# Performance work log

Measured on AMD Instinct MI355X. Metric: run time of the kernel, lower is better.

Reference implementation:

```python
import jax, jax.numpy as jnp
from jax import lax
import numpy as np

B = 256
EMB_DIM = 64
N_EMB = 512
LAT1 = 1024   # 16 slots * 64
LAT2 = 512
LAT = LAT1 + LAT2  # 1536
COMMIT = 0.25
EMB_COST = 1.0


def setup_inputs() -> dict:
    key = jax.random.key(0)
    ks = iter(jax.random.split(key, 40))

    def w(shape, fan_in):
        return jax.random.normal(next(ks), shape, jnp.float32) * np.float32(1.0 / np.sqrt(fan_in))

    def b(n):
        return jax.random.normal(next(ks), (n,), jnp.float32) * np.float32(0.01)

    inp = {}
    inp['x'] = jax.random.normal(next(ks), (B, 3, 64, 64), jnp.float32)
    # encoder convs, torch OIHW layout, k=4
    inp['ew0'] = w((64, 3, 4, 4), 3 * 16);   inp['eb0'] = b(64)
    inp['ew1'] = w((64, 64, 4, 4), 64 * 16); inp['eb1'] = b(64)
    inp['ew2'] = w((128, 64, 4, 4), 64 * 16); inp['eb2'] = b(128)
    inp['ew3'] = w((256, 128, 4, 4), 128 * 16); inp['eb3'] = b(256)
    # encoder fc11: 4096 -> 1024 -> 1024 -> 1536, stored (in,out)
    inp['fw0'] = w((4096, 1024), 4096); inp['fb0'] = b(1024)
    inp['fw1'] = w((1024, 1024), 1024); inp['fb1'] = b(1024)
    inp['fw2'] = w((1024, LAT), 1024);  inp['fb2'] = b(LAT)
    # VQ codebook
    inp['codebook'] = jax.random.normal(next(ks), (N_EMB, EMB_DIM), jnp.float32)
    # decoder fc3: 1536 -> 512 -> 1024 -> 4096
    inp['gw0'] = w((LAT, 512), LAT);    inp['gb0'] = b(512)
    inp['gw1'] = w((512, 1024), 512);   inp['gb1'] = b(1024)
    inp['gw2'] = w((1024, 4096), 1024); inp['gb2'] = b(4096)
    # decoder ConvTranspose2d weights, torch layout (Cin, Cout, kh, kw)
    inp['tw0'] = w((256, 128, 4, 4), 256 * 16); inp['tb0'] = b(128)
    inp['tw1'] = w((128, 64, 4, 4), 128 * 16);  inp['tb1'] = b(64)
    inp['tw2'] = w((64, 64, 4, 4), 64 * 16);    inp['tb2'] = b(64)
    inp['tw3'] = w((64, 3, 4, 4), 64 * 16);     inp['tb3'] = b(3)
    return inp


def _conv(x, w, b):
    # Conv2d k=4 s=2 p=1 -> halves H,W
    y = lax.conv_general_dilated(x, w, (2, 2), ((1, 1), (1, 1)),
                                 dimension_numbers=('NCHW', 'OIHW', 'NCHW'))
    return y + b[None, :, None, None]


def _convt(x, w, b):
    # ConvTranspose2d k=4 s=2 p=1 -> doubles H,W.
    # Equivalent to lhs_dilation=2, pad k-1-p=2, flipped kernel, swapped I/O.
    wf = jnp.flip(w, (2, 3)).transpose(1, 0, 2, 3)
    y = lax.conv_general_dilated(x, wf, (1, 1), ((2, 2), (2, 2)),
                                 lhs_dilation=(2, 2),
                                 dimension_numbers=('NCHW', 'OIHW', 'NCHW'))
    return y + b[None, :, None, None]


def _forward(x, ew0, eb0, ew1, eb1, ew2, eb2, ew3, eb3,
             fw0, fb0, fw1, fb1, fw2, fb2, codebook,
             gw0, gb0, gw1, gb1, gw2, gb2,
             tw0, tb0, tw1, tb1, tw2, tb2, tw3, tb3):
    relu = jax.nn.relu
    # --- encoder conv stack (last conv has no ReLU) ---
    h = relu(_conv(x, ew0, eb0))
    h = relu(_conv(h, ew1, eb1))
    h = relu(_conv(h, ew2, eb2))
    h = _conv(h, ew3, eb3)                      # [B,256,4,4]
    h = h.reshape(h.shape[0], -1)               # [B,4096]
    h = relu(h @ fw0 + fb0)
    h = relu(h @ fw1 + fb1)
    z = h @ fw2 + fb2                           # [B,1536]
    # --- split content / style (isVQStyle=False) ---
    z_c = z[:, :LAT1]
    z_s = z[:, LAT1:]
    # --- vector quantize z_c (16 slots of dim 64, shared codebook) ---
    flat = z_c.reshape(-1, EMB_DIM)             # [B*16, 64]
    d = (jnp.sum(flat * flat, axis=1, keepdims=True)
         + jnp.sum(codebook * codebook, axis=1)
         - 2.0 * flat @ codebook.T)             # [B*16, 512]
    idx = jnp.argmin(d, axis=1)
    quantized = codebook[idx].reshape(z_c.shape)  # [B,1024]
    sg = lax.stop_gradient
    q_latent_loss = jnp.mean((quantized - sg(z_c)) ** 2) * EMB_COST
    e_latent_loss = jnp.mean((z_c - sg(quantized)) ** 2) * COMMIT
    loss = q_latent_loss + e_latent_loss
    quantized = z_c + sg(quantized - z_c)       # straight-through
    e = jnp.concatenate([quantized, z_s], axis=-1)  # [B,1536]
    # --- decoder ---
    g = relu(e @ gw0 + gb0)
    g = relu(g @ gw1 + gb1)
    g = (g @ gw2 + gb2).reshape(-1, 256, 4, 4)
    g = relu(_convt(g, tw0, tb0))
    g = relu(_convt(g, tw1, tb1))
    g = relu(_convt(g, tw2, tb2))
    x_recon = _convt(g, tw3, tb3)               # [B,3,64,64]
    return x_recon, loss


def reference(x, ew0, eb0, ew1, eb1, ew2, eb2, ew3, eb3,
              fw0, fb0, fw1, fb1, fw2, fb2, codebook,
              gw0, gb0, gw1, gb1, gw2, gb2,
              tw0, tb0, tw1, tb1, tw2, tb2, tw3, tb3):
    return _forward(x, ew0, eb0, ew1, eb1, ew2, eb2, ew3, eb3,
                    fw0, fb0, fw1, fb1, fw2, fb2, codebook,
                    gw0, gb0, gw1, gb1, gw2, gb2,
                    tw0, tb0, tw1, tb1, tw2, tb2, tw3, tb3)
```

## Files before the change

### kernel.cpp

```cpp
#include <hip/hip_runtime.h>
#include <hip/hip_bf16.h>


#define TPB 256
typedef __attribute__((ext_vector_type(8))) short short8v;
typedef __attribute__((ext_vector_type(4))) float f32x4;
typedef unsigned int u32;
typedef unsigned short u16;

__device__ inline u16 f2bf(float x){
  union { __hip_bfloat16 b; u16 u; } cv;
  cv.b = __float2bfloat16(x);
  return cv.u;
}
__device__ inline float bf2f(u16 h){ union{u32 u;float f;}v; v.u=((u32)h)<<16; return v.f;}
__device__ inline u32 packhl(float x){ u16 h=f2bf(x); u16 l=f2bf(x-bf2f(h)); return ((u32)l<<16)|(u32)h;}

template<int NS>
__device__ inline void splitN(float x, u16 t[3]) {
  u16 h0 = f2bf(x); t[0] = h0;
  float r1 = x - bf2f(h0);
  u16 h1 = f2bf(r1); t[1] = h1;
  if (NS == 3) { float r2 = r1 - bf2f(h1); t[2] = f2bf(r2); }
}

template<int NS, int ST>
__device__ inline void stW(u32* L, int row, int oct, const u16 hs[3][8]) {
  constexpr int SWM = (ST == 64) ? 15 : 7;
  const int sw = row & SWM;
#pragma unroll
  for (int s = 0; s < NS; ++s) {
    uint4 d;
    d.x = (u32)hs[s][0] | ((u32)hs[s][1] << 16);
    d.y = (u32)hs[s][2] | ((u32)hs[s][3] << 16);
    d.z = (u32)hs[s][4] | ((u32)hs[s][5] << 16);
    d.w = (u32)hs[s][6] | ((u32)hs[s][7] << 16);
    int ch = (((s << 2) | oct) ^ sw) << 2;
    *reinterpret_cast<uint4*>(&L[row * ST + ch]) = d;
  }
}

template<int NS, int ST>
__device__ inline void stWf(u32* L, int row, int oct, const float v[8]) {
  u16 hs[3][8];
#pragma unroll
  for (int e = 0; e < 8; ++e) {
    u16 t3[3]; splitN<NS>(v[e], t3);
    hs[0][e] = t3[0]; hs[1][e] = t3[1]; if (NS == 3) hs[2][e] = t3[2];
  }
  stW<NS, ST>(L, row, oct, hs);
}

template<int ST>
__device__ inline void stWp(u32* L, int row, int oct, int s, uint4 d) {
  constexpr int SWM = (ST == 64) ? 15 : 7;
  int ch = (((s << 2) | oct) ^ (row & SWM)) << 2;
  *reinterpret_cast<uint4*>(&L[row * ST + ch]) = d;
}

template<int ST>
__device__ inline short8v rdFrag(const u32* L, int row, int c) {
  constexpr int SWM = (ST == 64) ? 15 : 7;
  int ph = (c ^ (row & SWM)) << 2;
  return *reinterpret_cast<const short8v*>(&L[row * ST + ph]);
}

__global__ __launch_bounds__(TPB) void wsplit3_k(
    const float* __restrict__ src, u16* __restrict__ dst, int n)
{
  for (int i = blockIdx.x * TPB + threadIdx.x; i < n; i += gridDim.x * TPB) {
    u16 t3[3]; splitN<3>(src[i], t3);
    dst[i] = t3[0]; dst[i + n] = t3[1]; dst[i + 2 * n] = t3[2];
  }
}
__global__ __launch_bounds__(TPB) void wprep2_k(
    const float* __restrict__ src, u16* __restrict__ dh, u16* __restrict__ dl,
    int Ci, int Co)
{
  int K4 = Ci << 2;
  int tot = 4 * Co * K4;
  for (int i = blockIdx.x * TPB + threadIdx.x; i < tot; i += gridDim.x * TPB) {
    int par = i / (Co * K4); int rem = i - par * (Co * K4);
    int co = rem / K4; int k4 = rem - co * K4;
    int ci = k4 >> 2, ay = (k4 >> 1) & 1, ax = k4 & 1;
    int py = par >> 1, px = par & 1;
    int widx = ((1 - py) << 2) + (1 - px) + (ay << 3) + (ax << 1);
    float x = src[(((size_t)ci * Co + co) << 4) + widx];
    u16 h = f2bf(x);
    dh[i] = h; dl[i] = f2bf(x - bf2f(h));
  }
}

__global__ __launch_bounds__(TPB) void x_pad_k(
    const float* __restrict__ x, float* __restrict__ xp)
{
  int idx = blockIdx.x * TPB + threadIdx.x;
  if (idx >= 3345408) return;
  int px = idx % 66; int t = idx / 66; int py = t % 66; int p = t / 66;
  float v = 0.f;
  if (py >= 1 && py <= 64 && px >= 1 && px <= 64)
    v = x[(size_t)p * 4096 + (py - 1) * 64 + (px - 1)];
  xp[idx] = v;
}
__global__ __launch_bounds__(TPB) void zb0_k(float* __restrict__ h0p)
{
  int idx = blockIdx.x * TPB + threadIdx.x;
  if (idx >= 2162688) return;
  int p = idx / 132, k = idx % 132;
  int py, px;
  if (k < 34)       { py = 0;           px = k; }
  else if (k < 68)  { py = 33;          px = k - 34; }
  else if (k < 100) { py = k - 68 + 1;  px = 0; }
  else              { py = k - 100 + 1; px = 33; }
  h0p[(size_t)p * 1156 + py * 34 + px] = 0.f;
}

template<int RM, int OUTM>
__global__ __launch_bounds__(TPB, 2) void conv_ad(
    const float* __restrict__ in, const u16* __restrict__ wsp,
    const float* __restrict__ bias, float* __restrict__ outp,
    int Ci, int Co, int Wi, int lwo, int relu, int KSPL, int PS,
    int bS, int ciS, int Mtot)
{
  constexpr int BM = RM * 64;
  __shared__ __align__(16) u32 BL[2][64 * 64];
  const int K = Ci << 4;
  const int PW = Wi + 2;
  const int Wo = Wi >> 1;
  const int tid = threadIdx.x;
  const int m0 = blockIdx.x * BM, n0 = blockIdx.y << 6;
  const int lane = tid & 63, wv = tid >> 6, r = lane & 15, g = lane >> 4;
  const int kb0 = blockIdx.z * KSPL;
  const int kbN = min(kb0 + KSPL, K);
  const int khsel = g & 1;
  const int cig = g >> 1;
  f32x4 acc[RM][4] = {};

  int base[RM];
#pragma unroll
  for (int mm = 0; mm < RM; ++mm) {
    int cell = m0 + (wv * RM + mm) * 16 + r;
    int x = cell & (Wo - 1), y = (cell >> lwo) & (Wo - 1), b = cell >> (lwo + lwo);
    base[mm] = b * bS + (2 * y + 2 * khsel) * PW + 2 * x;
  }

  auto gA = [&](int kb, float v[RM][8]) {
    if ((kb + (g << 3)) < K) {
      int cioff = ((kb >> 4) + cig) * ciS;
#pragma unroll
      for (int mm = 0; mm < RM; ++mm) {
        const float* p = in + base[mm] + cioff;
#pragma unroll
        for (int e = 0; e < 8; ++e)
          v[mm][e] = p[(e >> 2) * PW + (e & 3)];
      }
    } else {
#pragma unroll
      for (int mm = 0; mm < RM; ++mm)
#pragma unroll
        for (int e = 0; e < 8; ++e) v[mm][e] = 0.f;
    }
  };
  auto gB = [&](int kb, uint4* d) {
    int n = tid & 63, oc2 = tid >> 6;
    int k8 = kb + (oc2 << 3);
    if (k8 < K) {
      const u16* wp = wsp + (size_t)(n0 + n) * K + k8;
      d[0] = *reinterpret_cast<const uint4*>(wp);
      d[1] = *reinterpret_cast<const uint4*>(wp + PS);
      d[2] = *reinterpret_cast<const uint4*>(wp + 2 * PS);
    } else {
      d[0] = d[1] = d[2] = make_uint4(0u, 0u, 0u, 0u);
    }
  };
  auto mkfrags = [&](const float v[8], short8v f[3]) {
    u16 hs[3][8];
#pragma unroll
    for (int e = 0; e < 8; ++e) {
      u16 t3[3]; splitN<3>(v[e], t3);
      hs[0][e] = t3[0]; hs[1][e] = t3[1]; hs[2][e] = t3[2];
    }
#pragma unroll
    for (int s = 0; s < 3; ++s) {
      union { u16 u[8]; short8v sv; } cv;
#pragma unroll
      for (int e = 0; e < 8; ++e) cv.u[e] = hs[s][e];
      f[s] = cv.sv;
    }
  };

  float vA[RM][8], vA2[RM][8];
  uint4 vB[3], vB2[3];
  gA(kb0, vA); gB(kb0, vB);
  for (int kb = kb0; kb < kbN; kb += 32) {
    u32* BLc = BL[((kb - kb0) >> 5) & 1];
    {
      int n = tid & 63, oc2 = tid >> 6;
      stWp<64>(BLc, n, oc2, 0, vB[0]);
      stWp<64>(BLc, n, oc2, 1, vB[1]);
      stWp<64>(BLc, n, oc2, 2, vB[2]);
    }
    const bool more = (kb + 32) < kbN;
    if (more) { gB(kb + 32, vB2); gA(kb + 32, vA2); }
    short8v a_[RM][3];
#pragma unroll
    for (int mm = 0; mm < RM; ++mm) mkfrags(vA[mm], a_[mm]);
    __syncthreads();
#pragma unroll
    for (int ns = 0; ns < 4; ++ns) {
      short8v b_[3];
#pragma unroll
      for (int s = 0; s < 3; ++s) b_[s] = rdFrag<64>(BLc, (ns << 4) + r, (s << 2) | g);
#pragma unroll
      for (int mm = 0; mm < RM; ++mm) {
        acc[mm][ns] = __builtin_amdgcn_mfma_f32_16x16x32_bf16(a_[mm][0], b_[0], acc[mm][ns], 0, 0, 0);
        acc[mm][ns] = __builtin_amdgcn_mfma_f32_16x16x32_bf16(a_[mm][0], b_[1], acc[mm][ns], 0, 0, 0);
        acc[mm][ns] = __builtin_amdgcn_mfma_f32_16x16x32_bf16(a_[mm][1], b_[0], acc[mm][ns], 0, 0, 0);
        acc[mm][ns] = __builtin_amdgcn_mfma_f32_16x16x32_bf16(a_[mm][1], b_[1], acc[mm][ns], 0, 0, 0);
        acc[mm][ns] = __builtin_amdgcn_mfma_f32_16x16x32_bf16(a_[mm][0], b_[2], acc[mm][ns], 0, 0, 0);
        acc[mm][ns] = __builtin_amdgcn_mfma_f32_16x16x32_bf16(a_[mm][2], b_[0], acc[mm][ns], 0, 0, 0);
      }
    }
    if (more) {
#pragma unroll
      for (int mm = 0; mm < RM; ++mm)
#pragma unroll
        for (int e = 0; e < 8; ++e) vA[mm][e] = vA2[mm][e];
#pragma unroll
      for (int s = 0; s < 3; ++s) vB[s] = vB2[s];
    }
  }
#pragma unroll
  for (int mm = 0; mm < RM; ++mm)
#pragma unroll
    for (int ns = 0; ns < 4; ++ns) {
      int c0 = m0 + (wv * RM + mm) * 16 + (g << 2);
      int co = n0 + (ns << 4) + r;
      if (OUTM == 0) {
        float bv = bias[co];
        const int OPW = Wo + 2;
        const int OPHW = OPW * OPW;
#pragma unroll
        for (int q = 0; q < 4; ++q) {
          int cell = c0 + q;
          int x = cell & (Wo - 1), y = (cell >> lwo) & (Wo - 1), b = cell >> (lwo + lwo);
          float v = acc[mm][ns][q] + bv;
          if (relu) v = fmaxf(v, 0.f);
          outp[((size_t)(b * Co + co)) * OPHW + (y + 1) * OPW + (x + 1)] = v;
        }
      } else {
        float4 o;
        o.x = acc[mm][ns][0]; o.y = acc[mm][ns][1];
        o.z = acc[mm][ns][2]; o.w = acc[mm][ns][3];
        *reinterpret_cast<float4*>(
            &outp[((size_t)(blockIdx.z * Co + co)) * Mtot + c0]) = o;
      }
    }
}

__global__ __launch_bounds__(TPB) void combine_cm_k(
    const float* __restrict__ P, const float* __restrict__ bias,
    float* __restrict__ out)
{
  int idx = blockIdx.x * TPB + threadIdx.x;
  if (idx >= 5308416) return;
  int px = idx % 18; int t = idx / 18; int py = t % 18; t /= 18;
  int b = t % 256; int co = t / 256;
  float v = 0.f;
  if (py >= 1 && py <= 16 && px >= 1 && px <= 16) {
    int cell = b * 256 + (py - 1) * 16 + (px - 1);
    v = P[(size_t)co * 65536 + cell] + P[(size_t)(64 + co) * 65536 + cell] + bias[co];
    v = fmaxf(v, 0.f);
  }
  out[idx] = v;
}

__global__ __launch_bounds__(TPB) void combine_pad_k(
    const float* __restrict__ P, const float* __restrict__ bias,
    float* __restrict__ out)
{
  int idx = blockIdx.x * TPB + threadIdx.x;
  if (idx >= 3276800) return;
  int px = idx % 10; int t = idx / 10; int py = t % 10; t /= 10;
  int co = t % 128; int b = t / 128;
  float v = 0.f;
  if (py >= 1 && py <= 8 && px >= 1 && px <= 8) {
    int cell = b * 64 + (py - 1) * 8 + (px - 1);
    float s = 0.f;
#pragma unroll
    for (int z = 0; z < 4; ++z)
      s += P[((size_t)(z * 128 + co)) * 16384 + cell];
    v = fmaxf(s + bias[co], 0.f);
  }
  out[idx] = v;
}

__global__ __launch_bounds__(TPB) void conv_combine(
    const float* __restrict__ P, const float* __restrict__ bias,
    float* __restrict__ out, int Mtot, int N, int SK, int lwo, int relu)
{
  int idx = blockIdx.x * TPB + threadIdx.x;
  int mq = Mtot >> 2;
  int co = idx / mq;
  int cell0 = (idx - co * mq) << 2;
  if (co >= N) return;
  float4 s = make_float4(0.f, 0.f, 0.f, 0.f);
  for (int z = 0; z < SK; ++z) {
    const float4 pv = *reinterpret_cast<const float4*>(
        &P[((size_t)z * N + co) * Mtot + cell0]);
    s.x += pv.x; s.y += pv.y; s.z += pv.z; s.w += pv.w;
  }
  float bv = bias[co];
  s.x += bv; s.y += bv; s.z += bv; s.w += bv;
  if (relu) { s.x = fmaxf(s.x, 0.f); s.y = fmaxf(s.y, 0.f);
              s.z = fmaxf(s.z, 0.f); s.w = fmaxf(s.w, 0.f); }
  int Wo = 1 << lwo;
  int x = cell0 & (Wo - 1), y = (cell0 >> lwo) & (Wo - 1), b = cell0 >> (lwo + lwo);
  *reinterpret_cast<float4*>(&out[(((size_t)b * N + co) * Wo + y) * Wo + x]) = s;
}

template<int NS, int OUTM>
__global__ __launch_bounds__(TPB) void gemm_mf(
    const float* __restrict__ A, const float* __restrict__ W,
    const float* __restrict__ bias, void* __restrict__ outp,
    int M, int K, int N, int KSPL)
{
  constexpr int ST = (NS == 3) ? 64 : 32;
  __shared__ __align__(16) u32 L[(64 + 64) * ST];
  u32* AL = L; u32* BL = L + 64 * ST;
  const int tid = threadIdx.x;
  const int m0 = blockIdx.x << 6, n0 = blockIdx.y << 6;
  const int lane = tid & 63, wv = tid >> 6, r = lane & 15, g = lane >> 4;
  const int kb0 = blockIdx.z * KSPL;
  const int kbN = kb0 + KSPL;
  const int cl = tid & 63, oct = tid >> 6;
  f32x4 acc[4] = {};

  float vA[8], vB[8], vA2[8], vB2[8];
  auto gA = [&](int kt, float* v) {
    const float* ap = &A[(size_t)(m0 + cl) * K + kt + (oct << 3)];
    *reinterpret_cast<float4*>(&v[0]) = *reinterpret_cast<const float4*>(ap);
    *reinterpret_cast<float4*>(&v[4]) = *reinterpret_cast<const float4*>(ap + 4);
  };
  auto gB = [&](int kt, float* v) {
#pragma unroll
    for (int e = 0; e < 8; ++e)
      v[e] = W[(size_t)(kt + (oct << 3) + e) * N + n0 + cl];
  };

  gA(kb0, vA); gB(kb0, vB);
  for (int kt = kb0; kt < kbN; kt += 32) {
    const bool more = (kt + 32) < kbN;
    if (more) { gA(kt + 32, vA2); gB(kt + 32, vB2); }
    stWf<NS, ST>(AL, cl, oct, vA);
    stWf<NS, ST>(BL, cl, oct, vB);
    __syncthreads();
    short8v a_[3];
#pragma unroll
    for (int s = 0; s < NS; ++s) a_[s] = rdFrag<ST>(AL, (wv << 4) + r, (s << 2) | g);
#pragma unroll
    for (int ns = 0; ns < 4; ++ns) {
      short8v b_[3];
#pragma unroll
      for (int s = 0; s < NS; ++s) b_[s] = rdFrag<ST>(BL, (ns << 4) + r, (s << 2) | g);
      acc[ns] = __builtin_amdgcn_mfma_f32_16x16x32_bf16(a_[0], b_[0], acc[ns], 0, 0, 0);
      acc[ns] = __builtin_amdgcn_mfma_f32_16x16x32_bf16(a_[0], b_[1], acc[ns], 0, 0, 0);
      acc[ns] = __builtin_amdgcn_mfma_f32_16x16x32_bf16(a_[1], b_[0], acc[ns], 0, 0, 0);
      if (NS == 3) {
        acc[ns] = __builtin_amdgcn_mfma_f32_16x16x32_bf16(a_[1], b_[1], acc[ns], 0, 0, 0);
        acc[ns] = __builtin_amdgcn_mfma_f32_16x16x32_bf16(a_[0], b_[2], acc[ns], 0, 0, 0);
        acc[ns] = __builtin_amdgcn_mfma_f32_16x16x32_bf16(a_[2], b_[0], acc[ns], 0, 0, 0);
      }
    }
    __syncthreads();
    if (more) {
#pragma unroll
      for (int e = 0; e < 8; ++e) { vA[e] = vA2[e]; vB[e] = vB2[e]; }
    }
  }
#pragma unroll
  for (int ns = 0; ns < 4; ++ns)
#pragma unroll
    for (int q = 0; q < 4; ++q) {
      int m = m0 + (wv << 4) + (g << 2) + q;
      int n = n0 + (ns << 4) + r;
      float v = acc[ns][q];
      if (OUTM == 0) ((float*)outp)[((size_t)blockIdx.z * M + m) * N + n] = v;
      else           ((u32*)outp)[(size_t)m * N + n] = packhl(v + bias[n]);
    }
}

__global__ __launch_bounds__(TPB) void combine_k(
    const float* __restrict__ P, const float* __restrict__ bias,
    float* __restrict__ out, int MN, int N, int SK, int relu)
{
  int i4 = (blockIdx.x * TPB + threadIdx.x) << 2;
  if (i4 >= MN) return;
  float4 s = make_float4(0.f, 0.f, 0.f, 0.f);
  for (int z = 0; z < SK; ++z) {
    const float4 pv = *reinterpret_cast<const float4*>(&P[(size_t)z * MN + i4]);
    s.x += pv.x; s.y += pv.y; s.z += pv.z; s.w += pv.w;
  }
  int n = i4 % N;
  s.x += bias[n]; s.y += bias[n + 1]; s.z += bias[n + 2]; s.w += bias[n + 3];
  if (relu) { s.x = fmaxf(s.x, 0.f); s.y = fmaxf(s.y, 0.f);
              s.z = fmaxf(s.z, 0.f); s.w = fmaxf(s.w, 0.f); }
  *reinterpret_cast<float4*>(&out[i4]) = s;
}

__global__ __launch_bounds__(TPB) void combine_pk_k(
    const float* __restrict__ P, const float* __restrict__ bias,
    u32* __restrict__ out)
{
  int i4 = (blockIdx.x * TPB + threadIdx.x) << 2;
  if (i4 >= 1048576) return;
  const float4 p0 = *reinterpret_cast<const float4*>(&P[i4]);
  const float4 p1 = *reinterpret_cast<const float4*>(&P[1048576 + i4]);
  int n = i4 % 4096;
  uint4 o;
  o.x = packhl(p0.x + p1.x + bias[n]);
  o.y = packhl(p0.y + p1.y + bias[n + 1]);
  o.z = packhl(p0.z + p1.z + bias[n + 2]);
  o.w = packhl(p0.w + p1.w + bias[n + 3]);
  *reinterpret_cast<uint4*>(&out[i4]) = o;
}

template<int BM, int EMIT, int SPLITIN>
__global__ __launch_bounds__(TPB) void convt_mf2(
    const u32* __restrict__ in, const u16* __restrict__ wth,
    const u16* __restrict__ wtl, const float* __restrict__ bias,
    u32* __restrict__ outq, int Ci, int Co, int Hi, int lwi, int relu)
{
  constexpr int ST = 32, MS = BM / 64;
  constexpr int STC = BM + 4;
  constexpr int LSZ = ((BM + 64) * ST > 64 * STC) ? (BM + 64) * ST : 64 * STC;
  __shared__ __align__(16) u32 L[LSZ];
  u32* AL = L; u32* BL = L + BM * ST;
  const int Wi = Hi, K4 = Ci << 2;
  const int HW = Hi * Wi, HWq = HW >> 2, Wiq = Wi >> 1;
  const int par = blockIdx.z, py = par >> 1, px = par & 1;
  const int tid = threadIdx.x;
  const int m0 = blockIdx.x * BM, n0 = blockIdx.y << 6;
  const int lane = tid & 63, wv = tid >> 6, r = lane & 15, g = lane >> 4;
  f32x4 acc[MS][4] = {};

  const int cl  = (BM == 128) ? (tid & 127) : (tid & 63);
  const int oc0 = (BM == 128) ? (tid >> 7) : (tid >> 6);
  int offT[4]; u32 mskT[4];
  {
    int cell = m0 + cl;
    int X = cell & (Wi - 1), Y = (cell >> lwi) & (Wi - 1), b = cell >> (lwi + lwi);
#pragma unroll
    for (int t = 0; t < 4; ++t) {
      int ay = t >> 1, ax = t & 1;
      int gy = Y + py - ay, gx = X + px - ax;
      bool ok = (gy >= 0 && gy < Hi && gx >= 0 && gx < Wi);
      int gyc = min(max(gy, 0), Hi - 1), gxc = min(max(gx, 0), Wi - 1);
      if (SPLITIN) {
        int q = ((gyc & 1) << 1) | (gxc & 1);
        offT[t] = q * (256 * Ci * HWq) + b * Ci * HWq + (gyc >> 1) * Wiq + (gxc >> 1);
      } else {
        offT[t] = b * Ci * HW + gyc * Wi + gxc;
      }
      mskT[t] = ok ? 0xffffffffu : 0u;
    }
  }
  const int stepCi = SPLITIN ? HWq : HW;

  auto gA = [&](int kb, u32 v[][8]) {
#pragma unroll
    for (int p = 0; p < MS; ++p) {
      int oc = oc0 + (p << 1);
      int cibase = ((kb >> 2) + (oc << 1)) * stepCi;
#pragma unroll
      for (int e = 0; e < 8; ++e) {
        int t = e & 3;
        v[p][e] = in[offT[t] + cibase + ((e >> 2) ? stepCi : 0)] & mskT[t];
      }
    }
  };
  auto gB = [&](int kb, uint4* d) {
    int n = tid & 63, oc2 = tid >> 6;
    size_t base = (size_t)(par * Co + n0 + n) * K4 + kb + (oc2 << 3);
    d[0] = *reinterpret_cast<const uint4*>(wth + base);
    d[1] = *reinterpret_cast<const uint4*>(wtl + base);
  };

  u32 vA[MS][8], vA2[MS][8];
  uint4 vB[2], vB2[2];
  gA(0, vA); gB(0, vB);
  for (int kb = 0; kb < K4; kb += 32) {
    const bool more = (kb + 32) < K4;
    if (more) { gA(kb + 32, vA2); gB(kb + 32, vB2); }
#pragma unroll
    for (int p = 0; p < MS; ++p) {
      const u32* v = vA[p];
      const int sw = cl & 7;
      int oc = oc0 + (p << 1);
      uint4 dh, dl;
      dh.x = (v[0] & 0xffffu) | (v[1] << 16);  dl.x = (v[0] >> 16) | (v[1] & 0xffff0000u);
      dh.y = (v[2] & 0xffffu) | (v[3] << 16);  dl.y = (v[2] >> 16) | (v[3] & 0xffff0000u);
      dh.z = (v[4] & 0xffffu) | (v[5] << 16);  dl.z = (v[4] >> 16) | (v[5] & 0xffff0000u);
      dh.w = (v[6] & 0xffffu) | (v[7] << 16);  dl.w = (v[6] >> 16) | (v[7] & 0xffff0000u);
      *reinterpret_cast<uint4*>(&AL[cl * ST + ((oc ^ sw) << 2)]) = dh;
      *reinterpret_cast<uint4*>(&AL[cl * ST + (((4 | oc) ^ sw) << 2)]) = dl;
    }
    {
      int n = tid & 63, oc2 = tid >> 6;
      stWp<ST>(BL, n, oc2, 0, vB[0]);
      stWp<ST>(BL, n, oc2, 1, vB[1]);
    }
    __syncthreads();
    short8v a_[MS][2];
#pragma unroll
    for (int mm = 0; mm < MS; ++mm)
#pragma unroll
      for (int s = 0; s < 2; ++s)
        a_[mm][s] = rdFrag<ST>(AL, (wv * MS + mm) * 16 + r, (s << 2) | g);
#pragma unroll
    for (int ns = 0; ns < 4; ++ns) {
      short8v b_[2];
#pragma unroll
      for (int s = 0; s < 2; ++s) b_[s] = rdFrag<ST>(BL, (ns << 4) + r, (s << 2) | g);
#pragma unroll
      for (int mm = 0; mm < MS; ++mm) {
        acc[mm][ns] = __builtin_amdgcn_mfma_f32_16x16x32_bf16(a_[mm][0], b_[0], acc[mm][ns], 0, 0, 0);
        acc[mm][ns] = __builtin_amdgcn_mfma_f32_16x16x32_bf16(a_[mm][0], b_[1], acc[mm][ns], 0, 0, 0);
        acc[mm][ns] = __builtin_amdgcn_mfma_f32_16x16x32_bf16(a_[mm][1], b_[0], acc[mm][ns], 0, 0, 0);
      }
    }
    __syncthreads();
    if (more) {
#pragma unroll
      for (int p = 0; p < MS; ++p)
#pragma unroll
        for (int e = 0; e < 8; ++e) vA[p][e] = vA2[p][e];
      vB[0] = vB2[0]; vB[1] = vB2[1];
    }
  }
#pragma unroll
  for (int mm = 0; mm < MS; ++mm)
#pragma unroll
    for (int ns = 0; ns < 4; ++ns)
#pragma unroll
      for (int q = 0; q < 4; ++q) {
        int cell = (wv * MS + mm) * 16 + (g << 2) + q;
        int col = (ns << 4) + r;
        float v = acc[mm][ns][q] + bias[n0 + col];
        if (relu) v = fmaxf(v, 0.f);
        L[col * STC + cell] = EMIT ? packhl(v) : __float_as_uint(v);
      }
  __syncthreads();
  const size_t QO = (size_t)256 * Co * HW;
  u32* op = outq + (size_t)par * QO;
  constexpr int C4N = BM / 4;
  constexpr int NCH = (BM * 64) / (TPB * 4);
#pragma unroll
  for (int it = 0; it < NCH; ++it) {
    int lin = it * TPB + tid;
    int c4 = lin & (C4N - 1);
    int col = lin / C4N;
    int cell0 = c4 << 2;
    uint4 d = *reinterpret_cast<const uint4*>(&L[col * STC + cell0]);
    int gc = m0 + cell0;
    int Xo = gc & (Wi - 1), Yo = (gc >> lwi) & (Wi - 1), bo = gc >> (lwi + lwi);
    *reinterpret_cast<uint4*>(
        &op[((size_t)(bo * Co + n0 + col) * Hi + Yo) * Wi + Xo]) = d;
  }
}

__global__ __launch_bounds__(TPB) void convt3_kernel(
    const float* __restrict__ inq, const float* __restrict__ w,
    float* __restrict__ part)
{
  __shared__ float wl[3072];
  __shared__ float il[8][33 * 32];
  const int b = blockIdx.x;
  const int z = blockIdx.y;
  const int tid = threadIdx.x;
  for (int i = tid; i < 3072; i += TPB) wl[i] = w[i];
  const int Y = tid >> 3;
  const int X0 = (tid & 7) << 2;
  float acc[3][2][8];
#pragma unroll
  for (int o = 0; o < 3; ++o)
#pragma unroll
    for (int p = 0; p < 2; ++p)
#pragma unroll
      for (int q = 0; q < 8; ++q) acc[o][p][q] = 0.f;

  const int cbeg = z << 5, cend = cbeg + 32;
  for (int c0 = cbeg; c0 < cend; c0 += 8) {
    __syncthreads();
    for (int i = tid; i < 8192; i += TPB) {
      int cc = i >> 10, yy = (i >> 5) & 31, xx = i & 31;
      int q = ((yy & 1) << 1) | (xx & 1);
      il[cc][yy * 33 + xx] = inq[(size_t)q * 4194304 +
          (((size_t)b * 64 + c0 + cc) * 16 + (yy >> 1)) * 16 + (xx >> 1)];
    }
    __syncthreads();
    for (int cc = 0; cc < 8; ++cc) {
      float iv[3][6];
#pragma unroll
      for (int j = 0; j < 3; ++j) {
        int gy = Y - 1 + j;
        int gyc = min(max(gy, 0), 31);
        float my = (gy >= 0 && gy < 32) ? 1.f : 0.f;
#pragma unroll
        for (int k = 0; k < 6; ++k) {
          int gx = X0 - 1 + k;
          int gxc = min(max(gx, 0), 31);
          float mx = (gx >= 0 && gx < 32) ? 1.f : 0.f;
          iv[j][k] = il[cc][gyc * 33 + gxc] * (my * mx);
        }
      }
      const float* wq = &wl[(c0 + cc) * 48];
#pragma unroll
      for (int o = 0; o < 3; ++o) {
        const float* wo = wq + o * 16;
#pragma unroll
        for (int c = 0; c < 4; ++c) {
          acc[o][0][2*c]   = fmaf(iv[1][c+1], wo[5],  acc[o][0][2*c]);
          acc[o][0][2*c]   = fmaf(iv[1][c],   wo[7],  acc[o][0][2*c]);
          acc[o][0][2*c]   = fmaf(iv[0][c+1], wo[13], acc[o][0][2*c]);
          acc[o][0][2*c]   = fmaf(iv[0][c],   wo[15], acc[o][0][2*c]);
          acc[o][0][2*c+1] = fmaf(iv[1][c+2], wo[4],  acc[o][0][2*c+1]);
          acc[o][0][2*c+1] = fmaf(iv[1][c+1], wo[6],  acc[o][0][2*c+1]);
          acc[o][0][2*c+1] = fmaf(iv[0][c+2], wo[12], acc[o][0][2*c+1]);
          acc[o][0][2*c+1] = fmaf(iv[0][c+1], wo[14], acc[o][0][2*c+1]);
          acc[o][1][2*c]   = fmaf(iv[2][c+1], wo[1],  acc[o][1][2*c]);
          acc[o][1][2*c]   = fmaf(iv[2][c],   wo[3],  acc[o][1][2*c]);
          acc[o][1][2*c]   = fmaf(iv[1][c+1], wo[9],  acc[o][1][2*c]);
          acc[o][1][2*c]   = fmaf(iv[1][c],   wo[11], acc[o][1][2*c]);
          acc[o][1][2*c+1] = fmaf(iv[2][c+2], wo[0],  acc[o][1][2*c+1]);
          acc[o][1][2*c+1] = fmaf(iv[2][c+1], wo[2],  acc[o][1][2*c+1]);
          acc[o][1][2*c+1] = fmaf(iv[1][c+2], wo[8],  acc[o][1][2*c+1]);
          acc[o][1][2*c+1] = fmaf(iv[1][c+1], wo[10], acc[o][1][2*c+1]);
        }
      }
    }
  }
  float* pz = part + (size_t)z * 3145728;
#pragma unroll
  for (int o = 0; o < 3; ++o) {
#pragma unroll
    for (int p = 0; p < 2; ++p) {
      float* op = pz + (((size_t)b * 3 + o) * 64 + 2 * Y + p) * 64 + 2 * X0;
      *reinterpret_cast<float4*>(op) =
          make_float4(acc[o][p][0], acc[o][p][1], acc[o][p][2], acc[o][p][3]);
      *reinterpret_cast<float4*>(op + 4) =
          make_float4(acc[o][p][4], acc[o][p][5], acc[o][p][6], acc[o][p][7]);
    }
  }
}

__global__ __launch_bounds__(TPB) void c3_combine(
    const float* __restrict__ part, const float* __restrict__ bias,
    float* __restrict__ out)
{
  int i4 = (blockIdx.x * TPB + threadIdx.x) << 2;
  const float4 p0 = *reinterpret_cast<const float4*>(&part[i4]);
  const float4 p1 = *reinterpret_cast<const float4*>(&part[i4 + 3145728]);
  int o = (i4 >> 12) % 3;
  float bv = bias[o];
  float4 s = make_float4(p0.x + p1.x + bv, p0.y + p1.y + bv,
                         p0.z + p1.z + bv, p0.w + p1.w + bv);
  *reinterpret_cast<float4*>(&out[i4]) = s;
}

__global__ __launch_bounds__(TPB) void vq_kernel(
    const float* __restrict__ z, const float* __restrict__ cb,
    float* __restrict__ e, float* __restrict__ rowloss)
{
  const int row = blockIdx.x;
  const int b = row >> 4, s = row & 15;
  __shared__ float zr[64];
  __shared__ float bval[TPB];
  __shared__ int   bidx[TPB];
  const int tid = threadIdx.x;
  if (tid < 64) zr[tid] = z[(size_t)b * 1536 + s * 64 + tid];
  __syncthreads();

  float best = 3.4e38f;
  int bi = 0;
#pragma unroll
  for (int rep = 0; rep < 2; ++rep) {
    int j = tid + rep * TPB;
    const float4* c4 = reinterpret_cast<const float4*>(cb + (size_t)j * 64);
    float d = 0.f;
#pragma unroll
    for (int k = 0; k < 16; ++k) {
      float4 cv = c4[k];
      float t0 = zr[4 * k + 0] - cv.x;
      float t1 = zr[4 * k + 1] - cv.y;
      float t2 = zr[4 * k + 2] - cv.z;
      float t3 = zr[4 * k + 3] - cv.w;
      d = fmaf(t0, t0, d); d = fmaf(t1, t1, d);
      d = fmaf(t2, t2, d); d = fmaf(t3, t3, d);
    }
    if (d < best) { best = d; bi = j; }
  }
  bval[tid] = best; bidx[tid] = bi;
  __syncthreads();
  for (int sft = 128; sft > 0; sft >>= 1) {
    if (tid < sft) {
      float v2 = bval[tid + sft]; int i2 = bidx[tid + sft];
      if (v2 < bval[tid] || (v2 == bval[tid] && i2 < bidx[tid])) {
        bval[tid] = v2; bidx[tid] = i2;
      }
    }
    __syncthreads();
  }
  const int bj = bidx[0];
  if (tid < 64)
    e[(size_t)b * 1536 + s * 64 + tid] = cb[(size_t)bj * 64 + tid];
  if (tid == 0) rowloss[row] = bval[0];
}

__global__ __launch_bounds__(TPB) void zs_copy_kernel(
    const float* __restrict__ z, float* __restrict__ e)
{
  int i = blockIdx.x * TPB + threadIdx.x;
  int b = i >> 9, k = i & 511;
  e[(size_t)b * 1536 + 1024 + k] = z[(size_t)b * 1536 + 1024 + k];
}

__global__ __launch_bounds__(TPB) void loss_reduce_kernel(
    const float* __restrict__ rl, float* __restrict__ out)
{
  __shared__ float sm[TPB];
  float s = 0.f;
  for (int i = threadIdx.x; i < 4096; i += TPB) s += rl[i];
  sm[threadIdx.x] = s;
  __syncthreads();
  for (int sft = 128; sft > 0; sft >>= 1) {
    if (threadIdx.x < sft) sm[threadIdx.x] += sm[threadIdx.x + sft];
    __syncthreads();
  }
  if (threadIdx.x == 0) out[0] = sm[0] * (1.25f / 262144.f);
}

extern "C" void kernel_launch(void* const* d_in, const int* in_sizes, int n_in,
                              void* d_out, int out_size, void* d_ws, size_t ws_size,
                              hipStream_t stream)
{
  const float* x    = (const float*)d_in[0];
  const float* ew0  = (const float*)d_in[1];
  const float* eb0  = (const float*)d_in[2];
  const float* ew1  = (const float*)d_in[3];
  const float* eb1  = (const float*)d_in[4];
  const float* ew2  = (const float*)d_in[5];
  const float* eb2  = (const float*)d_in[6];
  const float* ew3  = (const float*)d_in[7];
  const float* eb3  = (const float*)d_in[8];
  const float* fw0  = (const float*)d_in[9];
  const float* fb0  = (const float*)d_in[10];
  const float* fw1  = (const float*)d_in[11];
  const float* fb1  = (const float*)d_in[12];
  const float* fw2  = (const float*)d_in[13];
  const float* fb2  = (const float*)d_in[14];
  const float* cb   = (const float*)d_in[15];
  const float* gw0  = (const float*)d_in[16];
  const float* gb0  = (const float*)d_in[17];
  const float* gw1  = (const float*)d_in[18];
  const float* gb1  = (const float*)d_in[19];
  const float* gw2  = (const float*)d_in[20];
  const float* gb2  = (const float*)d_in[21];
  const float* tw0  = (const float*)d_in[22];
  const float* tb0  = (const float*)d_in[23];
  const float* tw1  = (const float*)d_in[24];
  const float* tb1  = (const float*)d_in[25];
  const float* tw2  = (const float*)d_in[26];
  const float* tb2  = (const float*)d_in[27];
  const float* tw3  = (const float*)d_in[28];
  const float* tb3  = (const float*)d_in[29];

  float* out = (float*)d_out;
  float* ws  = (float*)d_ws;

  u16*   WE0  = (u16*)(ws + 0);
  u16*   WE1  = (u16*)(ws + 4608);
  u16*   WE2  = (u16*)(ws + 102912);
  u16*   WE3  = (u16*)(ws + 299520);
  float* RL   = ws + 1085952;
  float* H0P  = ws + 1090048;
  float* PC1  = ws + 20029952;
  float* XP   = ws + 20029952;
  float* H1P  = ws + 1090048;
  float* PC23 = ws + 6398464;
  float* H2P  = ws + 14787072;
  float* H3   = ws + 18063872;
  float* P    = ws + 1090048;
  float* F0   = ws + 5284352;
  float* F1   = ws + 5546496;
  float* Z    = ws + 5808640;
  float* E    = ws + 6201856;
  float* G0   = ws + 6595072;
  float* G1   = ws + 6726144;
  float* T2S  = ws + 1090048;
  u16*   WT0h = (u16*)(ws + 17867264);
  u16*   WT0l = (u16*)(ws + 18129408);
  u16*   WT1h = (u16*)(ws + 18391552);
  u16*   WT1l = (u16*)(ws + 18457088);
  u16*   WT2h = (u16*)(ws + 18522624);
  u16*   WT2l = (u16*)(ws + 18555392);
  float* PG2  = ws + 18588160;
  u32*   G2P  = (u32*)(ws + 20685312);
  u32*   T0S  = (u32*)(ws + 21733888);
  u32*   T1S  = (u32*)(ws + 23831040);
  float* PT3  = ws + 18588160;

  wsplit3_k<<<dim3(12),  TPB, 0, stream>>>(ew0, WE0, 3072);
  wsplit3_k<<<dim3(256), TPB, 0, stream>>>(ew1, WE1, 65536);
  wsplit3_k<<<dim3(512), TPB, 0, stream>>>(ew2, WE2, 131072);
  wsplit3_k<<<dim3(1024),TPB, 0, stream>>>(ew3, WE3, 524288);
  x_pad_k<<<dim3(13068), TPB, 0, stream>>>(x, XP);
  zb0_k<<<dim3(8448), TPB, 0, stream>>>(H0P);

  conv_ad<4,0><<<dim3(1024, 1, 1), TPB, 0, stream>>>(
      XP, WE0, eb0, H0P, 3, 64, 64, 5, 1, 48, 3072, 13068, 4356, 0);
  conv_ad<4,1><<<dim3(256, 1, 2), TPB, 0, stream>>>(
      H0P, WE1, eb1, PC1, 64, 64, 32, 4, 1, 512, 65536, 73984, 1156, 65536);
  combine_cm_k<<<dim3(20736), TPB, 0, stream>>>(PC1, eb1, H1P);
  conv_ad<4,1><<<dim3(64, 2, 4), TPB, 0, stream>>>(
      H1P, WE2, eb2, PC23, 64, 128, 16, 3, 1, 256, 131072, 324, 82944, 16384);
  combine_pad_k<<<dim3(12800), TPB, 0, stream>>>(PC23, eb2, H2P);
  conv_ad<4,1><<<dim3(16, 4, 8), TPB, 0, stream>>>(
      H2P, WE3, eb3, PC23, 128, 256, 8, 2, 0, 256, 524288, 12800, 100, 4096);
  conv_combine<<<dim3(1024), TPB, 0, stream>>>(PC23, eb3, H3, 4096, 256, 8, 2, 0);

  gemm_mf<3,0><<<dim3(4, 16, 16), TPB, 0, stream>>>(H3, fw0, fb0, (void*)P, 256, 4096, 1024, 256);
  combine_k<<<dim3(256), TPB, 0, stream>>>(P, fb0, F0, 262144, 1024, 16, 1);
  gemm_mf<3,0><<<dim3(4, 16, 8), TPB, 0, stream>>>(F0, fw1, fb1, (void*)P, 256, 1024, 1024, 128);
  combine_k<<<dim3(256), TPB, 0, stream>>>(P, fb1, F1, 262144, 1024, 8, 1);
  gemm_mf<3,0><<<dim3(4, 24, 8), TPB, 0, stream>>>(F1, fw2, fb2, (void*)P, 256, 1024, 1536, 128);
  combine_k<<<dim3(384), TPB, 0, stream>>>(P, fb2, Z, 393216, 1536, 8, 0);

  vq_kernel<<<dim3(4096), TPB, 0, stream>>>(Z, cb, E, RL);
  zs_copy_kernel<<<dim3(512), TPB, 0, stream>>>(Z, E);
  loss_reduce_kernel<<<dim3(1), TPB, 0, stream>>>(RL, out + (size_t)out_size - 1);

  gemm_mf<2,0><<<dim3(4, 8, 8), TPB, 0, stream>>>(E,  gw0, gb0, (void*)P, 256, 1536, 512, 192);
  combine_k<<<dim3(128), TPB, 0, stream>>>(P, gb0, G0, 131072, 512, 8, 1);
  gemm_mf<2,0><<<dim3(4, 16, 4), TPB, 0, stream>>>(G0, gw1, gb1, (void*)P, 256, 512, 1024, 128);
  combine_k<<<dim3(256), TPB, 0, stream>>>(P, gb1, G1, 262144, 1024, 4, 1);

  wprep2_k<<<dim3(512), TPB, 0, stream>>>(tw0, WT0h, WT0l, 256, 128);
  wprep2_k<<<dim3(128), TPB, 0, stream>>>(tw1, WT1h, WT1l, 128, 64);
  wprep2_k<<<dim3(64),  TPB, 0, stream>>>(tw2, WT2h, WT2l, 64, 64);

  gemm_mf<2,0><<<dim3(4, 64, 2), TPB, 0, stream>>>(G1, gw2, gb2, (void*)PG2, 256, 1024, 4096, 512);
  combine_pk_k<<<dim3(1024), TPB, 0, stream>>>(PG2, gb2, G2P);

  convt_mf2<64,1,0><<<dim3(64, 2, 4),   TPB, 0, stream>>>(G2P, WT0h, WT0l, tb0, T0S, 256, 128, 4,  2, 1);
  convt_mf2<128,1,1><<<dim3(128, 1, 4), TPB, 0, stream>>>(T0S, WT1h, WT1l, tb1, T1S, 128, 64,  8,  3, 1);
  convt_mf2<128,0,1><<<dim3(512, 1, 4), TPB, 0, stream>>>(T1S, WT2h, WT2l, tb2, (u32*)T2S, 64, 64, 16, 4, 1);
  convt3_kernel<<<dim3(256, 2), TPB, 0, stream>>>(T2S, tw3, PT3);
  c3_combine<<<dim3(3072), TPB, 0, stream>>>(PT3, tb3, out);
}
```

Measured before the change: 565.0 us.

## Batch VQ rows per block with LDS codebook tiles; split convt epilogue LDS

The VQ kernel now handles 8 latent rows per block instead of one. It stages 64-codeword codebook tiles transposed into LDS, and each wave computes distances for two rows, reducing the argmin with wavefront shuffles instead of a shared-memory tree. This cuts redundant codebook reads from global memory and removes many block-wide barriers. Separately, the convt epilogue writes its output through LDS in two 32-column phases, so the shared buffer can shrink to the main-loop size, which may help occupancy at the cost of extra barriers.

```diff
diff --git a/kernel.cpp b/kernel.cpp
--- a/kernel.cpp
+++ b/kernel.cpp
@@ -433,7 +433,8 @@
 {
   constexpr int ST = 32, MS = BM / 64;
   constexpr int STC = BM + 4;
-  constexpr int LSZ = ((BM + 64) * ST > 64 * STC) ? (BM + 64) * ST : 64 * STC;
+  constexpr int LSZ = (BM + 64) * ST;
+  static_assert(32 * STC <= LSZ, "epilogue phase must fit main LDS");
   __shared__ __align__(16) u32 L[LSZ];
   u32* AL = L; u32* BL = L + BM * ST;
   const int Wi = Hi, K4 = Ci << 2;
@@ -538,34 +539,41 @@
       vB[0] = vB2[0]; vB[1] = vB2[1];
     }
   }
-#pragma unroll
-  for (int mm = 0; mm < MS; ++mm)
-#pragma unroll
-    for (int ns = 0; ns < 4; ++ns)
-#pragma unroll
-      for (int q = 0; q < 4; ++q) {
-        int cell = (wv * MS + mm) * 16 + (g << 2) + q;
-        int col = (ns << 4) + r;
-        float v = acc[mm][ns][q] + bias[n0 + col];
-        if (relu) v = fmaxf(v, 0.f);
-        L[col * STC + cell] = EMIT ? packhl(v) : __float_as_uint(v);
-      }
-  __syncthreads();
   const size_t QO = (size_t)256 * Co * HW;
   u32* op = outq + (size_t)par * QO;
   constexpr int C4N = BM / 4;
-  constexpr int NCH = (BM * 64) / (TPB * 4);
-#pragma unroll
-  for (int it = 0; it < NCH; ++it) {
-    int lin = it * TPB + tid;
-    int c4 = lin & (C4N - 1);
-    int col = lin / C4N;
-    int cell0 = c4 << 2;
-    uint4 d = *reinterpret_cast<const uint4*>(&L[col * STC + cell0]);
-    int gc = m0 + cell0;
-    int Xo = gc & (Wi - 1), Yo = (gc >> lwi) & (Wi - 1), bo = gc >> (lwi + lwi);
-    *reinterpret_cast<uint4*>(
-        &op[((size_t)(bo * Co + n0 + col) * Hi + Yo) * Wi + Xo]) = d;
+  constexpr int NCH = (BM * 32) / (TPB * 4);
+#pragma unroll
+  for (int ph = 0; ph < 2; ++ph) {
+    __syncthreads();
+#pragma unroll
+    for (int mm = 0; mm < MS; ++mm)
+#pragma unroll
+      for (int nn = 0; nn < 2; ++nn) {
+        int ns = (ph << 1) + nn;
+#pragma unroll
+        for (int q = 0; q < 4; ++q) {
+          int cell = (wv * MS + mm) * 16 + (g << 2) + q;
+          int colL = (nn << 4) + r;
+          float v = acc[mm][ns][q] + bias[n0 + (ph << 5) + colL];
+          if (relu) v = fmaxf(v, 0.f);
+          L[colL * STC + cell] = EMIT ? packhl(v) : __float_as_uint(v);
+        }
+      }
+    __syncthreads();
+#pragma unroll
+    for (int it = 0; it < NCH; ++it) {
+      int lin = it * TPB + tid;
+      int c4 = lin & (C4N - 1);
+      int colL = lin / C4N;
+      int col = (ph << 5) + colL;
+      int cell0 = c4 << 2;
+      uint4 d = *reinterpret_cast<const uint4*>(&L[colL * STC + cell0]);
+      int gc = m0 + cell0;
+      int Xo = gc & (Wi - 1), Yo = (gc >> lwi) & (Wi - 1), bo = gc >> (lwi + lwi);
+      *reinterpret_cast<uint4*>(
+          &op[((size_t)(bo * Co + n0 + col) * Hi + Yo) * Wi + Xo]) = d;
+    }
   }
 }
 
@@ -668,53 +676,67 @@
   *reinterpret_cast<float4*>(&out[i4]) = s;
 }
 
-__global__ __launch_bounds__(TPB) void vq_kernel(
+__global__ __launch_bounds__(TPB) void vq8_kernel(
     const float* __restrict__ z, const float* __restrict__ cb,
     float* __restrict__ e, float* __restrict__ rowloss)
 {
-  const int row = blockIdx.x;
-  const int b = row >> 4, s = row & 15;
-  __shared__ float zr[64];
-  __shared__ float bval[TPB];
-  __shared__ int   bidx[TPB];
+  __shared__ float cbL[64][65];
+  __shared__ float zr[8][64];
   const int tid = threadIdx.x;
-  if (tid < 64) zr[tid] = z[(size_t)b * 1536 + s * 64 + tid];
-  __syncthreads();
-
-  float best = 3.4e38f;
-  int bi = 0;
+  const int lane = tid & 63, wid = tid >> 6;
+  const int r0 = blockIdx.x << 3;
+
+  for (int i = tid; i < 512; i += TPB) {
+    int rr = i >> 6, k = i & 63;
+    int row = r0 + rr;
+    int b = row >> 4, s = row & 15;
+    zr[rr][k] = z[(size_t)b * 1536 + s * 64 + k];
+  }
+
+  float best[2] = {3.4e38f, 3.4e38f};
+  int bi[2] = {0, 0};
+
+  for (int c0 = 0; c0 < 512; c0 += 64) {
+    __syncthreads();
+#pragma unroll
+    for (int i = 0; i < 4; ++i) {
+      int j = (tid >> 4) + (i << 4);
+      int kq = tid & 15;
+      const float4 v = *reinterpret_cast<const float4*>(
+          &cb[(size_t)(c0 + j) * 64 + (kq << 2)]);
+      cbL[(kq << 2) + 0][j] = v.x;
+      cbL[(kq << 2) + 1][j] = v.y;
+      cbL[(kq << 2) + 2][j] = v.z;
+      cbL[(kq << 2) + 3][j] = v.w;
+    }
+    __syncthreads();
+#pragma unroll
+    for (int rep = 0; rep < 2; ++rep) {
+      const float* zp = zr[wid + (rep << 2)];
+      float d = 0.f;
+#pragma unroll
+      for (int k = 0; k < 64; ++k) {
+        float t = zp[k] - cbL[k][lane];
+        d = fmaf(t, t, d);
+      }
+      if (d < best[rep]) { best[rep] = d; bi[rep] = c0 + lane; }
+    }
+  }
 #pragma unroll
   for (int rep = 0; rep < 2; ++rep) {
-    int j = tid + rep * TPB;
-    const float4* c4 = reinterpret_cast<const float4*>(cb + (size_t)j * 64);
-    float d = 0.f;
-#pragma unroll
-    for (int k = 0; k < 16; ++k) {
-      float4 cv = c4[k];
-      float t0 = zr[4 * k + 0] - cv.x;
-      float t1 = zr[4 * k + 1] - cv.y;
-      float t2 = zr[4 * k + 2] - cv.z;
-      float t3 = zr[4 * k + 3] - cv.w;
-      d = fmaf(t0, t0, d); d = fmaf(t1, t1, d);
-      d = fmaf(t2, t2, d); d = fmaf(t3, t3, d);
-    }
-    if (d < best) { best = d; bi = j; }
-  }
-  bval[tid] = best; bidx[tid] = bi;
-  __syncthreads();
-  for (int sft = 128; sft > 0; sft >>= 1) {
-    if (tid < sft) {
-      float v2 = bval[tid + sft]; int i2 = bidx[tid + sft];
-      if (v2 < bval[tid] || (v2 == bval[tid] && i2 < bidx[tid])) {
-        bval[tid] = v2; bidx[tid] = i2;
-      }
-    }
-    __syncthreads();
-  }
-  const int bj = bidx[0];
-  if (tid < 64)
-    e[(size_t)b * 1536 + s * 64 + tid] = cb[(size_t)bj * 64 + tid];
-  if (tid == 0) rowloss[row] = bval[0];
+#pragma unroll
+    for (int off = 32; off > 0; off >>= 1) {
+      float ob = __shfl_xor(best[rep], off);
+      int   oi = __shfl_xor(bi[rep], off);
+      if (ob < best[rep] || (ob == best[rep] && oi < bi[rep])) {
+        best[rep] = ob; bi[rep] = oi;
+      }
+    }
+    int row = r0 + wid + (rep << 2);
+    int b = row >> 4, s = row & 15;
+    e[(size_t)b * 1536 + s * 64 + lane] = cb[(size_t)bi[rep] * 64 + lane];
+    if (lane == 0) rowloss[row] = best[rep];
+  }
 }
 
 __global__ __launch_bounds__(TPB) void zs_copy_kernel(
@@ -836,7 +858,7 @@
   gemm_mf<3,0><<<dim3(4, 24, 8), TPB, 0, stream>>>(F1, fw2, fb2, (void*)P, 256, 1024, 1536, 128);
   combine_k<<<dim3(384), TPB, 0, stream>>>(P, fb2, Z, 393216, 1536, 8, 0);
 
-  vq_kernel<<<dim3(4096), TPB, 0, stream>>>(Z, cb, E, RL);
+  vq8_kernel<<<dim3(512), TPB, 0, stream>>>(Z, cb, E, RL);
   zs_copy_kernel<<<dim3(512), TPB, 0, stream>>>(Z, E);
   loss_reduce_kernel<<<dim3(1), TPB, 0, stream>>>(RL, out + (size_t)out_size - 1);
 
```

Measured after the change: 532.0 us. -5.8%, faster.
